# Optimization experiments

Hardware: AMD Instinct MI355X
Metric: run time of the kernel (lower is better)

Reference implementation:

```python
import jax, jax.numpy as jnp
import numpy as np

C = 1.0          # ball curvature c (manifold k = -c)
RC = 1.0         # sqrt(c)
PROJ_EPS = 4e-3  # geoopt float32 projection eps
NUM_HEADS = 16
B, S, D = 2, 1024, 1024


def _project(x):
    # clip points back inside the Poincare ball
    maxnorm = (1.0 - PROJ_EPS) / RC
    norm = jnp.maximum(jnp.linalg.norm(x, axis=-1, keepdims=True), 1e-15)
    return jnp.where(norm > maxnorm, x / norm * maxnorm, x)


def _poincare_linear(x, z, r, out_split):
    # Unidirectional Poincare MLR (Shimizu et al., HNN++) followed by exp-map back to the ball.
    # x: [..., din]; z: [din, dout]; r: [dout]
    z_norm = jnp.maximum(jnp.linalg.norm(z, axis=0, keepdims=True), 1e-15)  # [1, dout]
    z_unit = z / z_norm
    drcr = 2.0 * RC * r                                    # [dout]
    rcx = RC * x
    cx2 = jnp.sum(rcx * rcx, axis=-1, keepdims=True)       # [..., 1]
    w = 2.0 * (z_norm / RC) * jnp.arcsinh(
        (2.0 * (rcx @ z_unit) * jnp.cosh(drcr) - (1.0 + cx2) * jnp.sinh(drcr))
        / jnp.maximum(1.0 - cx2, 1e-15))
    y = jnp.sinh(RC * w) / RC
    y = y.reshape(y.shape[:-1] + (out_split, y.shape[-1] // out_split))  # [..., H, dh]
    y = _project(y)
    y = y / (1.0 + jnp.sqrt(1.0 + C * jnp.sum(y * y, axis=-1, keepdims=True)))
    return _project(y)


def _dist_matmul(x, y):
    # Pairwise Poincare distance via matmul. x: [..., n, d], y: [..., d, m].
    # dist = (1/sqrt(c)) * arccosh(1 + 2c||x-y||^2 / ((1-c||x||^2)(1-c||y||^2)))
    xy = jnp.matmul(x, y)
    x2 = jnp.sum(x * x, axis=-1, keepdims=True)           # [..., n, 1]
    y2 = jnp.sum(y * y, axis=-2, keepdims=True)           # [..., 1, m]
    num = jnp.maximum(x2 - 2.0 * xy + y2, 1e-15)          # ||x - y||^2
    den = jnp.maximum((1.0 - C * x2) * (1.0 - C * y2), 1e-15)
    return (1.0 / RC) * jnp.arccosh(1.0 + 2.0 * C * num / den)


def _weighted_midpoint_bmm(xs, weights):
    # Weighted Mobius gyromidpoint. xs: [..., n, d], weights: [..., m, n] -> [..., m, d]
    x2 = jnp.sum(xs * xs, axis=-1, keepdims=True)
    gamma = 2.0 / jnp.maximum(1.0 - C * x2, 1e-15)        # conformal factor lambda_x
    denom = jnp.matmul(jnp.abs(weights), gamma - 1.0)     # [..., m, 1]
    nomin = jnp.matmul(weights, gamma * xs)               # [..., m, d]
    two_mean = nomin / jnp.maximum(denom, 1e-10)
    sq = jnp.sum(two_mean * two_mean, axis=-1, keepdims=True)
    a_mean = two_mean / (1.0 + jnp.sqrt(jnp.maximum(1.0 - C * sq, 1e-15)))
    return _project(a_mean)


def setup_inputs() -> dict:
    key = jax.random.key(0)
    ks = jax.random.split(key, 4)
    # points must lie inside the unit ball: ||x|| ~ 0.02*sqrt(D) ~ 0.64
    hidden_states = 0.02 * jax.random.normal(ks[0], (B, S, D), dtype=jnp.float32)
    attention_mask = jnp.zeros((B, 1, 1, S), dtype=jnp.float32)
    scale = 1.0 / np.sqrt(D).astype(np.float32)
    qz = scale * jax.random.normal(ks[1], (D, D), dtype=jnp.float32)
    kz = scale * jax.random.normal(ks[2], (D, D), dtype=jnp.float32)
    vz = scale * jax.random.normal(ks[3], (D, D), dtype=jnp.float32)
    qr = jnp.zeros((D,), jnp.float32)
    kr = jnp.zeros((D,), jnp.float32)
    vr = jnp.zeros((D,), jnp.float32)
    return {"hidden_states": hidden_states, "attention_mask": attention_mask,
            "qz": qz, "qr": qr, "kz": kz, "kr": kr, "vz": vz, "vr": vr}


def reference(hidden_states, attention_mask, qz, qr, kz, kr, vz, vr):
    # self-attention path (encoder_hidden_states is None), eval mode (dropout p=0)
    q = _poincare_linear(hidden_states, qz, qr, NUM_HEADS).transpose(0, 2, 1, 3)  # [B,H,S,dh]
    k = _poincare_linear(hidden_states, kz, kr, NUM_HEADS).transpose(0, 2, 1, 3)
    v = _poincare_linear(hidden_states, vz, vr, NUM_HEADS).transpose(0, 2, 1, 3)
    scores = -_dist_matmul(q, jnp.swapaxes(k, -1, -2)) + attention_mask          # [B,H,S,S]
    probs = jax.nn.softmax(scores, axis=-1)
    ctx = _weighted_midpoint_bmm(v, probs)                                       # [B,H,S,dh]
    b, h, s, dh = ctx.shape
    return ctx.transpose(0, 2, 1, 3).reshape(b, s, h * dh)
```

## Files before the change

### kernel.cpp

```cpp
#include <hip/hip_runtime.h>
#include <math.h>

#define BB 2
#define SS 1024
#define DD 1024
#define NH 16
#define DH 64
#define MAXN 0.996f

typedef __attribute__((ext_vector_type(8))) short bf16x8;
typedef __attribute__((ext_vector_type(4))) float f32x4;

__device__ __forceinline__ float xor_sum16(float v){
  v += __shfl_xor(v, 1, 64);
  v += __shfl_xor(v, 2, 64);
  v += __shfl_xor(v, 4, 64);
  v += __shfl_xor(v, 8, 64);
  return v;
}

__device__ __forceinline__ unsigned short f2bf(float x){
  unsigned u = __builtin_bit_cast(unsigned, x);
  unsigned r = u + 0x7FFFu + ((u >> 16) & 1u);
  return (unsigned short)(r >> 16);
}
__device__ __forceinline__ float bf2f(unsigned short b){
  unsigned u = ((unsigned)b) << 16;
  return __builtin_bit_cast(float, u);
}

__device__ __forceinline__ void async_copy16(const unsigned short* g, unsigned short* s){
  __builtin_amdgcn_global_load_lds(
      (const __attribute__((address_space(1))) unsigned int*)g,
      (__attribute__((address_space(3))) unsigned int*)s,
      16, 0, 0);
}

__global__ __launch_bounds__(256) void prep_kernel(
    const float* __restrict__ hs,
    const float* __restrict__ zq, const float* __restrict__ zk, const float* __restrict__ zv,
    float* __restrict__ cx2, float* __restrict__ partial,
    unsigned short* __restrict__ Xhi, unsigned short* __restrict__ Xlo,
    unsigned short* __restrict__ ZThi, unsigned short* __restrict__ ZTlo)
{
  __shared__ unsigned shbuf[64 * 69];
  __shared__ float csred[4][64];
  const int bid = blockIdx.x;
  const int tid = threadIdx.x;

  if (bid < 1024) {
    const int b = bid;
    const size_t g0 = (size_t)b * 2048 + (size_t)tid * 8;
    float acc = 0.0f;
    #pragma unroll
    for (int h = 0; h < 2; ++h) {
      float4 v = *(const float4*)(hs + g0 + 4 * h);
      float a[4] = {v.x, v.y, v.z, v.w};
      ushort4 hv, lv;
      unsigned short* hp = (unsigned short*)&hv;
      unsigned short* lp = (unsigned short*)&lv;
      #pragma unroll
      for (int j = 0; j < 4; ++j) {
        acc = fmaf(a[j], a[j], acc);
        unsigned short hi = f2bf(a[j]);
        hp[j] = hi;
        lp[j] = f2bf(a[j] - bf2f(hi));
      }
      *(ushort4*)(Xhi + g0 + 4 * h) = hv;
      *(ushort4*)(Xlo + g0 + 4 * h) = lv;
    }
    #pragma unroll
    for (int m = 1; m < 64; m <<= 1) acc += __shfl_xor(acc, m, 64);
    float* red = (float*)shbuf;
    const int wave = tid >> 6, lane = tid & 63;
    if (lane == 0) red[wave] = acc;
    __syncthreads();
    if (tid == 0)   cx2[2 * b]     = red[0] + red[1];
    if (tid == 128) cx2[2 * b + 1] = red[2] + red[3];
  } else {
    const int b2 = bid - 1024;
    const int kt = b2 & 15, nt = (b2 >> 4) & 15, mat = b2 >> 8;
    const float* z = (mat == 0) ? zq : ((mat == 1) ? zk : zv);
    const int wave = tid >> 6, lane = tid & 63;
    unsigned (*T)[69] = (unsigned(*)[69])shbuf;
    float cs[4] = {0.f, 0.f, 0.f, 0.f};
    #pragma unroll
    for (int i = 0; i < 4; ++i) {
      const int g = tid + 256 * i;
      const int kr = g >> 4, nc = (g & 15) * 4;
      float4 v = *(const float4*)(z + (size_t)(kt * 64 + kr) * DD + nt * 64 + nc);
      float a[4] = {v.x, v.y, v.z, v.w};
      #pragma unroll
      for (int j = 0; j < 4; ++j) {
        cs[j] = fmaf(a[j], a[j], cs[j]);
        unsigned short hi = f2bf(a[j]);
        unsigned short lo = f2bf(a[j] - bf2f(hi));
        T[kr][nc + j] = ((unsigned)lo << 16) | (unsigned)hi;
      }
    }
    #pragma unroll
    for (int j = 0; j < 4; ++j) {
      cs[j] += __shfl_xor(cs[j], 16, 64);
      cs[j] += __shfl_xor(cs[j], 32, 64);
    }
    if (lane < 16) {
      #pragma unroll
      for (int j = 0; j < 4; ++j) csred[wave][lane * 4 + j] = cs[j];
    }
    __syncthreads();
    #pragma unroll
    for (int i = 0; i < 4; ++i) {
      const int g = tid + 256 * i;
      const int nr = g >> 4, kc = (g & 15) * 4;
      ushort4 hv, lv;
      unsigned short* hp = (unsigned short*)&hv;
      unsigned short* lp = (unsigned short*)&lv;
      #pragma unroll
      for (int j = 0; j < 4; ++j) {
        unsigned u = T[kc + j][nr];
        hp[j] = (unsigned short)(u & 0xFFFFu);
        lp[j] = (unsigned short)(u >> 16);
      }
      const size_t ob = ((size_t)mat * DD + nt * 64 + nr) * DD + kt * 64 + kc;
      *(ushort4*)(ZThi + ob) = hv;
      *(ushort4*)(ZTlo + ob) = lv;
    }
    if (tid < 64) {
      float s = csred[0][tid] + csred[1][tid] + csred[2][tid] + csred[3][tid];
      partial[kt * 3072 + mat * DD + nt * 64 + tid] = s;
    }
  }
}

__global__ __launch_bounds__(256) void colstats_finalize_kernel(
    const float* __restrict__ partial,
    const float* __restrict__ rq, const float* __restrict__ rk, const float* __restrict__ rv,
    float* __restrict__ acol, float* __restrict__ bcol, float* __restrict__ scol)
{
  const int col = blockIdx.x * 256 + threadIdx.x;
  float s = 0.f;
  #pragma unroll
  for (int rc = 0; rc < 16; ++rc) s += partial[rc * 3072 + col];
  const int m = col >> 10, c = col & 1023;
  const float* r = (m == 0) ? rq : ((m == 1) ? rk : rv);
  const float n = fmaxf(sqrtf(s), 1e-15f);
  const float rr = 2.0f * r[c];
  acol[col] = 2.0f * coshf(rr) / n;
  bcol[col] = sinhf(rr);
  scol[col] = 2.0f * n;
}

__global__ __launch_bounds__(256, 2) void gemm_mfma_kernel(
    const unsigned short* __restrict__ Xhi, const unsigned short* __restrict__ Xlo,
    const unsigned short* __restrict__ ZThi, const unsigned short* __restrict__ ZTlo,
    const float* __restrict__ acol, const float* __restrict__ bcol, const float* __restrict__ scol,
    const float* __restrict__ cx2,
    unsigned short* __restrict__ Qhi, unsigned short* __restrict__ Qlo,
    unsigned short* __restrict__ Khi, unsigned short* __restrict__ Klo,
    unsigned short* __restrict__ GThi, unsigned short* __restrict__ GTlo,
    float* __restrict__ q2, float* __restrict__ k2, float* __restrict__ gm1)
{
  __shared__ __align__(16) unsigned char shmem[66560];
  unsigned short* Sbuf = (unsigned short*)shmem;

  const int mat = blockIdx.z;
  float* Stat = (mat == 0) ? q2 : ((mat == 1) ? k2 : gm1);
  unsigned short* Bh = (mat == 0) ? Qhi : Khi;
  unsigned short* Bl = (mat == 0) ? Qlo : Klo;

  const int n0 = blockIdx.x * 128;
  const int m0 = blockIdx.y * 128;
  const int tid = threadIdx.x;
  const int wave = tid >> 6, lane = tid & 63;
  const int tx = lane & 15, quad = lane >> 4;
  const int wrow = wave >> 1;
  const int wcol = wave & 1;

  const int l4r = lane >> 2;
  const int l4c = 8 * (((lane & 3) - (l4r >> 1)) & 3);
  const unsigned short* abase =
      (wave == 0) ? Xhi : (wave == 1) ? Xlo : (wave == 2) ? ZThi : ZTlo;
  const size_t rowbase = (wave < 2) ? (size_t)m0 : (size_t)(mat * DD + n0);
  const unsigned short* P[8];
  #pragma unroll
  for (int i = 0; i < 8; ++i)
    P[i] = abase + (rowbase + i * 16 + l4r) * DD + l4c;
  const int ldsw = 4096 * wave;

  const int koff = 8 * ((quad + (tx >> 1)) & 3);

  const f32x4 z4 = {0.f, 0.f, 0.f, 0.f};
  f32x4 acc[4][4];
  #pragma unroll
  for (int mb = 0; mb < 4; ++mb)
    #pragma unroll
    for (int nb = 0; nb < 4; ++nb) acc[mb][nb] = z4;

  #pragma unroll
  for (int i = 0; i < 8; ++i) {
    async_copy16(P[i], Sbuf + ldsw + 512 * i);
    P[i] += 32;
  }

  for (int kt = 0; kt < 32; ++kt) {
    __syncthreads();
    if (kt < 31) {
      unsigned short* Bn = Sbuf + 16384 * ((kt + 1) & 1);
      #pragma unroll
      for (int i = 0; i < 8; ++i) {
        async_copy16(P[i], Bn + ldsw + 512 * i);
        P[i] += 32;
      }
    }
    const unsigned short* Bc = Sbuf + 16384 * (kt & 1);

    bf16x8 a_h[4], a_l[4];
    #pragma unroll
    for (int mb = 0; mb < 4; ++mb) {
      const int ar = 64 * wrow + 16 * mb + tx;
      a_h[mb] = *(const bf16x8*)&Bc[ar * 32 + koff];
      a_l[mb] = *(const bf16x8*)&Bc[4096 + ar * 32 + koff];
    }
    #pragma unroll
    for (int nb = 0; nb < 4; ++nb) {
      const int br = 64 * wcol + 16 * nb + tx;
      bf16x8 b_h = *(const bf16x8*)&Bc[8192 + br * 32 + koff];
      bf16x8 b_l = *(const bf16x8*)&Bc[12288 + br * 32 + koff];
      #pragma unroll
      for (int mb = 0; mb < 4; ++mb)
        acc[mb][nb] = __builtin_amdgcn_mfma_f32_16x16x32_bf16(a_h[mb], b_h, acc[mb][nb], 0, 0, 0);
      #pragma unroll
      for (int mb = 0; mb < 4; ++mb)
        acc[mb][nb] = __builtin_amdgcn_mfma_f32_16x16x32_bf16(a_h[mb], b_l, acc[mb][nb], 0, 0, 0);
      #pragma unroll
      for (int mb = 0; mb < 4; ++mb)
        acc[mb][nb] = __builtin_amdgcn_mfma_f32_16x16x32_bf16(a_l[mb], b_h, acc[mb][nb], 0, 0, 0);
    }
  }

  const int head = blockIdx.x * 2 + wcol;
  unsigned* Tr = (unsigned*)shmem;
  if (mat == 2) __syncthreads();

  #pragma unroll
  for (int mb = 0; mb < 4; ++mb) {
    #pragma unroll
    for (int r = 0; r < 4; ++r) {
      const int sl = 64 * wrow + 16 * mb + 4 * quad + r;
      const int row = m0 + sl;
      const float c2 = cx2[row];
      const float inv = 1.0f / fmaxf(1.0f - c2, 1e-15f);
      const float onec = 1.0f + c2;
      float yv[4];
      #pragma unroll
      for (int nb = 0; nb < 4; ++nb) {
        const float accv = acc[mb][nb][r];
        const int col = mat * DD + n0 + 64 * wcol + 16 * nb + tx;
        const float u = fmaf(accv, acol[col], -(onec * bcol[col])) * inv;
        const float a = fabsf(u);
        const float t = a + sqrtf(fmaf(a, a, 1.0f));
        const float p = __builtin_amdgcn_exp2f(scol[col] * __builtin_amdgcn_logf(t));
        float y = 0.5f * (p - __builtin_amdgcn_rcpf(p));
        yv[nb] = copysignf(y, u);
      }
      const int b = row >> 10, s = row & 1023;
      float n2 = 0.f;
      #pragma unroll
      for (int j = 0; j < 4; ++j) n2 = fmaf(yv[j], yv[j], n2);
      n2 = xor_sum16(n2);
      float n = fmaxf(sqrtf(n2), 1e-15f);
      float s1 = (n > MAXN) ? (MAXN / n) : 1.0f;
      n2 = n2 * s1 * s1;
      float f = 1.0f / (1.0f + sqrtf(1.0f + n2));
      float fs = s1 * f;
      n2 = n2 * f * f;
      float nb2 = fmaxf(sqrtf(n2), 1e-15f);
      float s2f = (nb2 > MAXN) ? (MAXN / nb2) : 1.0f;
      fs *= s2f;
      n2 = n2 * s2f * s2f;

      const size_t bh = (size_t)(b * NH + head);
      const size_t outbase = (bh * SS + s) * DH;
      if (mat == 2) {
        const float gamma = 2.0f / fmaxf(1.0f - n2, 1e-15f);
        #pragma unroll
        for (int j = 0; j < 4; ++j) {
          const float v = yv[j] * fs * gamma;
          const unsigned short hi = f2bf(v);
          const unsigned short lo = f2bf(v - bf2f(hi));
          Tr[(wcol * 128 + sl) * 65 + 16 * j + tx] = ((unsigned)lo << 16) | (unsigned)hi;
        }
        if (tx == 0) Stat[bh * SS + s] = gamma - 1.0f;
      } else {
        #pragma unroll
        for (int j = 0; j < 4; ++j) {
          const float v = yv[j] * fs;
          const unsigned short hi = f2bf(v);
          const unsigned short lo = f2bf(v - bf2f(hi));
          Bh[outbase + 16 * j + tx] = hi;
          Bl[outbase + 16 * j + tx] = lo;
        }
        if (tx == 0) Stat[bh * SS + s] = n2;
      }
    }
  }

  if (mat == 2) {
    __syncthreads();
    const int bb = m0 >> 10, sbase = m0 & 1023;
    #pragma unroll
    for (int i = 0; i < 4; ++i) {
      const int task = tid + 256 * i;
      const int rowid = task >> 3;
      const int hh = rowid >> 6, dh = rowid & 63;
      const int sc = (task & 7) * 16;
      unsigned short hbuf[16] __attribute__((aligned(16)));
      unsigned short lbuf[16] __attribute__((aligned(16)));
      #pragma unroll
      for (int s = 0; s < 16; ++s) {
        unsigned u = Tr[(hh * 128 + sc + s) * 65 + dh];
        hbuf[s] = (unsigned short)(u & 0xFFFFu);
        lbuf[s] = (unsigned short)(u >> 16);
      }
      const int hg = blockIdx.x * 2 + hh;
      const size_t ob = (((size_t)(bb * NH + hg)) * DH + dh) * SS + sbase + sc;
      *(uint4*)(GThi + ob)     = *(uint4*)&hbuf[0];
      *(uint4*)(GThi + ob + 8) = *(uint4*)&hbuf[8];
      *(uint4*)(GTlo + ob)     = *(uint4*)&lbuf[0];
      *(uint4*)(GTlo + ob + 8) = *(uint4*)&lbuf[8];
    }
  }
}

__global__ __launch_bounds__(256) void flash_attn_kernel(
    const unsigned short* __restrict__ Qhi, const unsigned short* __restrict__ Qlo,
    const unsigned short* __restrict__ Khi, const unsigned short* __restrict__ Klo,
    const unsigned short* __restrict__ GThi, const unsigned short* __restrict__ GTlo,
    const float* __restrict__ q2a, const float* __restrict__ k2a, const float* __restrict__ gm1a,
    const float* __restrict__ mask, float* __restrict__ out)
{
  __shared__ unsigned short Ksh[2][2048];
  __shared__ unsigned short Ksl[2][2048];
  __shared__ unsigned short Gsh[2][2048];
  __shared__ unsigned short Gsl[2][2048];
  __shared__ unsigned short Psh[64 * 40];
  __shared__ unsigned short Psl[64 * 40];
  __shared__ float k2s[2][32], ik2s[2][32], gm1s[2][32], ems[2][32];

  const int h = blockIdx.x, qt = blockIdx.y, b = blockIdx.z;
  const int bh = b * NH + h;
  const int tid = threadIdx.x;
  const int wave = tid >> 6, lane = tid & 63;
  const int tx = lane & 15, quad = lane >> 4;
  const int r0 = qt * 64;

  bf16x8 qa_h[2], qa_l[2];
  {
    const size_t qoff = ((size_t)bh * SS + r0 + 16 * wave + tx) * DH;
    #pragma unroll
    for (int kc = 0; kc < 2; ++kc) {
      qa_h[kc] = *(const bf16x8*)(Qhi + qoff + 32 * kc + 8 * quad);
      qa_l[kc] = *(const bf16x8*)(Qlo + qoff + 32 * kc + 8 * quad);
    }
  }
  float q2r[4], iq2[4];
  #pragma unroll
  for (int r = 0; r < 4; ++r) {
    q2r[r] = q2a[(size_t)bh * SS + r0 + 16 * wave + 4 * quad + r];
    iq2[r] = 2.0f / fmaxf(1.0f - q2r[r], 1e-15f);
  }

  const f32x4 zero4 = {0.f, 0.f, 0.f, 0.f};
  f32x4 oacc[4] = {zero4, zero4, zero4, zero4};
  float dden[4] = {0.f, 0.f, 0.f, 0.f};

  const size_t kbase = (size_t)bh * SS * DH;
  const size_t gbase = (size_t)bh * DH * SS;

  const unsigned short* sArr =
      (wave == 0) ? Khi : (wave == 1) ? Klo : (wave == 2) ? GThi : GTlo;
  const unsigned short* sBase = sArr + ((wave < 2) ? kbase : gbase);
  const int tAdv = (wave < 2) ? 32 * DH : 32;
  int srcoff[4];
  if (wave < 2) {
    #pragma unroll
    for (int i = 0; i < 4; ++i) {
      const int r = 8 * i + (lane >> 3);
      srcoff[i] = r * DH + 8 * (((lane & 7) - r) & 7);
    }
  } else {
    #pragma unroll
    for (int i = 0; i < 4; ++i) {
      const int r = 16 * i + (lane >> 2);
      srcoff[i] = r * SS + 8 * (((lane & 3) - r) & 3);
    }
  }
  unsigned short* ldsDst[2];
  ldsDst[0] = (wave == 0) ? Ksh[0] : (wave == 1) ? Ksl[0] : (wave == 2) ? Gsh[0] : Gsl[0];
  ldsDst[1] = (wave == 0) ? Ksh[1] : (wave == 1) ? Ksl[1] : (wave == 2) ? Gsh[1] : Gsl[1];

  float s_k2 = 0.f, s_gm1 = 0.f, s_ms = 0.f;

  {
    const unsigned short* s = sBase;
    #pragma unroll
    for (int i = 0; i < 4; ++i) async_copy16(s + srcoff[i], ldsDst[0] + i * 512);
  }
  if (tid < 32) {
    s_k2  = k2a[(size_t)bh * SS + tid];
    s_gm1 = gm1a[(size_t)bh * SS + tid];
    s_ms  = mask[(size_t)b * SS + tid];
    k2s[0][tid]  = s_k2;
    ik2s[0][tid] = 1.0f / fmaxf(1.0f - s_k2, 1e-15f);
    gm1s[0][tid] = s_gm1;
    ems[0][tid]  = __expf(s_ms);
    s_k2  = k2a[(size_t)bh * SS + 32 + tid];
    s_gm1 = gm1a[(size_t)bh * SS + 32 + tid];
    s_ms  = mask[(size_t)b * SS + 32 + tid];
  }

  for (int kt = 0; kt < 32; ++kt) {
    __syncthreads();
    if (kt < 31) {
      const int nbuf = (kt + 1) & 1;
      const unsigned short* s = sBase + (size_t)(kt + 1) * tAdv;
      #pragma unroll
      for (int i = 0; i < 4; ++i) async_copy16(s + srcoff[i], ldsDst[nbuf] + i * 512);
      if (tid < 32) {
        k2s[nbuf][tid]  = s_k2;
        ik2s[nbuf][tid] = 1.0f / fmaxf(1.0f - s_k2, 1e-15f);
        gm1s[nbuf][tid] = s_gm1;
        ems[nbuf][tid]  = __expf(s_ms);
        if (kt < 30) {
          const int t2 = (kt + 2) * 32;
          s_k2  = k2a[(size_t)bh * SS + t2 + tid];
          s_gm1 = gm1a[(size_t)bh * SS + t2 + tid];
          s_ms  = mask[(size_t)b * SS + t2 + tid];
        }
      }
    }
    const int cb = kt & 1;

    f32x4 sacc[2] = {zero4, zero4};
    #pragma unroll
    for (int kc = 0; kc < 2; ++kc) {
      #pragma unroll
      for (int nb = 0; nb < 2; ++nb) {
        const int row = 16 * nb + tx;
        const int off = row * 64 + 8 * (((4 * kc + quad) + row) & 7);
        bf16x8 kh = *(const bf16x8*)&Ksh[cb][off];
        bf16x8 kl = *(const bf16x8*)&Ksl[cb][off];
        sacc[nb] = __builtin_amdgcn_mfma_f32_16x16x32_bf16(qa_h[kc], kh, sacc[nb], 0, 0, 0);
        sacc[nb] = __builtin_amdgcn_mfma_f32_16x16x32_bf16(qa_h[kc], kl, sacc[nb], 0, 0, 0);
        sacc[nb] = __builtin_amdgcn_mfma_f32_16x16x32_bf16(qa_l[kc], kh, sacc[nb], 0, 0, 0);
      }
    }

    float pb[4][2];
    #pragma unroll
    for (int nb = 0; nb < 2; ++nb) {
      const int key = 16 * nb + tx;
      const float k2v = k2s[cb][key], ikv = ik2s[cb][key], emv = ems[cb][key], gmv = gm1s[cb][key];
      #pragma unroll
      for (int r = 0; r < 4; ++r) {
        float sv = sacc[nb][r];
        float num = fmaxf(fmaf(-2.0f, sv, q2r[r] + k2v), 1e-15f);
        float e = num * iq2[r] * ikv;
        float g = fmaf(e, e, e + e);
        float z = 1.0f + e + __builtin_amdgcn_sqrtf(g);
        float w = emv * __builtin_amdgcn_rcpf(z);
        pb[r][nb] = w;
        dden[r] = fmaf(w, gmv, dden[r]);
      }
    }

    #pragma unroll
    for (int r = 0; r < 4; ++r) {
      const int prow = 16 * wave + 4 * quad + r;
      #pragma unroll
      for (int nb = 0; nb < 2; ++nb) {
        float w = pb[r][nb];
        unsigned short hi = f2bf(w);
        unsigned short lo = f2bf(w - bf2f(hi));
        Psh[prow * 40 + 16 * nb + tx] = hi;
        Psl[prow * 40 + 16 * nb + tx] = lo;
      }
    }
    bf16x8 ph = *(const bf16x8*)&Psh[(16 * wave + tx) * 40 + 8 * quad];
    bf16x8 pl = *(const bf16x8*)&Psl[(16 * wave + tx) * 40 + 8 * quad];
    #pragma unroll
    for (int nb = 0; nb < 4; ++nb) {
      const int row = 16 * nb + tx;
      const int off = row * 32 + 8 * ((quad + row) & 3);
      bf16x8 gh = *(const bf16x8*)&Gsh[cb][off];
      bf16x8 gl = *(const bf16x8*)&Gsl[cb][off];
      oacc[nb] = __builtin_amdgcn_mfma_f32_16x16x32_bf16(ph, gh, oacc[nb], 0, 0, 0);
      oacc[nb] = __builtin_amdgcn_mfma_f32_16x16x32_bf16(ph, gl, oacc[nb], 0, 0, 0);
      oacc[nb] = __builtin_amdgcn_mfma_f32_16x16x32_bf16(pl, gh, oacc[nb], 0, 0, 0);
    }
  }

  #pragma unroll
  for (int r = 0; r < 4; ++r) {
    float d = fmaxf(xor_sum16(dden[r]), 1e-10f);
    float invd = 1.0f / d;
    float tm[4]; float sq = 0.f;
    #pragma unroll
    for (int nb = 0; nb < 4; ++nb) { tm[nb] = oacc[nb][r] * invd; sq = fmaf(tm[nb], tm[nb], sq); }
    sq = xor_sum16(sq);
    const float f = 1.0f / (1.0f + sqrtf(fmaxf(1.0f - sq, 1e-15f)));
    const float n2 = sq * f * f;
    const float n = fmaxf(sqrtf(n2), 1e-15f);
    const float s2 = (n > MAXN) ? (MAXN / n) : 1.0f;
    const float fs = f * s2;
    const int qrow = r0 + 16 * wave + 4 * quad + r;
    #pragma unroll
    for (int nb = 0; nb < 4; ++nb)
      out[((size_t)(b * SS + qrow)) * DD + h * DH + 16 * nb + tx] = tm[nb] * fs;
  }
}

extern "C" void kernel_launch(void* const* d_in, const int* in_sizes, int n_in,
                              void* d_out, int out_size, void* d_ws, size_t ws_size,
                              hipStream_t stream) {
  const float* hs   = (const float*)d_in[0];
  const float* mask = (const float*)d_in[1];
  const float* qz   = (const float*)d_in[2];
  const float* qr   = (const float*)d_in[3];
  const float* kz   = (const float*)d_in[4];
  const float* kr   = (const float*)d_in[5];
  const float* vz   = (const float*)d_in[6];
  const float* vr   = (const float*)d_in[7];
  float* out = (float*)d_out;

  float* ws = (float*)d_ws;
  const size_t nQKV = (size_t)BB * NH * SS * DH;
  const size_t nStat = (size_t)BB * NH * SS;

  float* q2  = ws;
  float* k2  = q2 + nStat;
  float* gm1 = k2 + nStat;
  float* acol = gm1 + nStat;
  float* bcol = acol + 3 * DD;
  float* scol = bcol + 3 * DD;
  float* cx2 = scol + 3 * DD;
  float* partial = cx2 + 2048;

  unsigned short* sb   = (unsigned short*)(partial + 16 * 3072);
  unsigned short* Qhi  = sb;
  unsigned short* Qlo  = Qhi + nQKV;
  unsigned short* Khi  = Qlo + nQKV;
  unsigned short* Klo  = Khi + nQKV;
  unsigned short* GThi = Klo + nQKV;
  unsigned short* GTlo = GThi + nQKV;
  unsigned short* Xhi  = GTlo + nQKV;
  unsigned short* Xlo  = Xhi + nQKV;
  unsigned short* ZThi = Xlo + nQKV;
  unsigned short* ZTlo = ZThi + 3 * (size_t)DD * DD;

  prep_kernel<<<dim3(1792), 256, 0, stream>>>(
      hs, qz, kz, vz, cx2, partial, Xhi, Xlo, ZThi, ZTlo);
  colstats_finalize_kernel<<<dim3(12), 256, 0, stream>>>(
      partial, qr, kr, vr, acol, bcol, scol);
  gemm_mfma_kernel<<<dim3(8, 16, 3), 256, 0, stream>>>(
      Xhi, Xlo, ZThi, ZTlo, acol, bcol, scol, cx2,
      Qhi, Qlo, Khi, Klo, GThi, GTlo, q2, k2, gm1);
  flash_attn_kernel<<<dim3(NH, 16, BB), 256, 0, stream>>>(
      Qhi, Qlo, Khi, Klo, GThi, GTlo, q2, k2, gm1, mask, out);
}
```

Baseline: 200.2 us.

## Fuse GEMM and flash attention into one cooperative kernel with grid sync

Drops the separate column-stats finalize kernel by computing the per-column coefficients inside the GEMM epilogue. The GEMM and attention stages are merged into one cooperative launch of 512 blocks that does a grid-wide sync between them, with a fallback to two separate launches if the cooperative launch fails. The aim is to remove launch overheads and inter-kernel gaps. In exchange, every GEMM block now redundantly re-reads the partial sums, and the attention phase runs with the GEMM's larger shared-memory footprint and occupancy bound of 2 blocks per CU.

```diff
diff --git a/kernel.cpp b/kernel.cpp
--- a/kernel.cpp
+++ b/kernel.cpp
@@ -1,5 +1,8 @@
 #include <hip/hip_runtime.h>
+#include <hip/hip_cooperative_groups.h>
 #include <math.h>
+
+namespace cg = cooperative_groups;
 
 #define BB 2
 #define SS 1024
@@ -132,44 +135,26 @@
   }
 }
 
-__global__ __launch_bounds__(256) void colstats_finalize_kernel(
+__device__ __forceinline__ void gemm_body(
+    int bx, int by, int mat, unsigned char* shmem,
+    const unsigned short* __restrict__ Xhi, const unsigned short* __restrict__ Xlo,
+    const unsigned short* __restrict__ ZThi, const unsigned short* __restrict__ ZTlo,
     const float* __restrict__ partial,
     const float* __restrict__ rq, const float* __restrict__ rk, const float* __restrict__ rv,
-    float* __restrict__ acol, float* __restrict__ bcol, float* __restrict__ scol)
-{
-  const int col = blockIdx.x * 256 + threadIdx.x;
-  float s = 0.f;
-  #pragma unroll
-  for (int rc = 0; rc < 16; ++rc) s += partial[rc * 3072 + col];
-  const int m = col >> 10, c = col & 1023;
-  const float* r = (m == 0) ? rq : ((m == 1) ? rk : rv);
-  const float n = fmaxf(sqrtf(s), 1e-15f);
-  const float rr = 2.0f * r[c];
-  acol[col] = 2.0f * coshf(rr) / n;
-  bcol[col] = sinhf(rr);
-  scol[col] = 2.0f * n;
-}
-
-__global__ __launch_bounds__(256, 2) void gemm_mfma_kernel(
-    const unsigned short* __restrict__ Xhi, const unsigned short* __restrict__ Xlo,
-    const unsigned short* __restrict__ ZThi, const unsigned short* __restrict__ ZTlo,
-    const float* __restrict__ acol, const float* __restrict__ bcol, const float* __restrict__ scol,
     const float* __restrict__ cx2,
     unsigned short* __restrict__ Qhi, unsigned short* __restrict__ Qlo,
     unsigned short* __restrict__ Khi, unsigned short* __restrict__ Klo,
     unsigned short* __restrict__ GThi, unsigned short* __restrict__ GTlo,
     float* __restrict__ q2, float* __restrict__ k2, float* __restrict__ gm1)
 {
-  __shared__ __align__(16) unsigned char shmem[66560];
   unsigned short* Sbuf = (unsigned short*)shmem;
 
-  const int mat = blockIdx.z;
   float* Stat = (mat == 0) ? q2 : ((mat == 1) ? k2 : gm1);
   unsigned short* Bh = (mat == 0) ? Qhi : Khi;
   unsigned short* Bl = (mat == 0) ? Qlo : Klo;
 
-  const int n0 = blockIdx.x * 128;
-  const int m0 = blockIdx.y * 128;
+  const int n0 = bx * 128;
+  const int m0 = by * 128;
   const int tid = threadIdx.x;
   const int wave = tid >> 6, lane = tid & 63;
   const int tx = lane & 15, quad = lane >> 4;
@@ -238,7 +223,25 @@
     }
   }
 
-  const int head = blockIdx.x * 2 + wcol;
+  float acolv[4], bcolv[4], scolv[4];
+  {
+    const float* rarr = (mat == 0) ? rq : ((mat == 1) ? rk : rv);
+    #pragma unroll
+    for (int nb = 0; nb < 4; ++nb) {
+      const int c = n0 + 64 * wcol + 16 * nb + tx;
+      const int colg = mat * DD + c;
+      float s = 0.f;
+      #pragma unroll
+      for (int rc = 0; rc < 16; ++rc) s += partial[rc * 3072 + colg];
+      const float n = fmaxf(sqrtf(s), 1e-15f);
+      const float rr2 = 2.0f * rarr[c];
+      acolv[nb] = 2.0f * coshf(rr2) / n;
+      bcolv[nb] = sinhf(rr2);
+      scolv[nb] = 2.0f * n;
+    }
+  }
+
+  const int head = bx * 2 + wcol;
   unsigned* Tr = (unsigned*)shmem;
   if (mat == 2) __syncthreads();
 
@@ -255,11 +258,10 @@
       #pragma unroll
       for (int nb = 0; nb < 4; ++nb) {
         const float accv = acc[mb][nb][r];
-        const int col = mat * DD + n0 + 64 * wcol + 16 * nb + tx;
-        const float u = fmaf(accv, acol[col], -(onec * bcol[col])) * inv;
+        const float u = fmaf(accv, acolv[nb], -(onec * bcolv[nb])) * inv;
         const float a = fabsf(u);
         const float t = a + sqrtf(fmaf(a, a, 1.0f));
-        const float p = __builtin_amdgcn_exp2f(scol[col] * __builtin_amdgcn_logf(t));
+        const float p = __builtin_amdgcn_exp2f(scolv[nb] * __builtin_amdgcn_logf(t));
         float y = 0.5f * (p - __builtin_amdgcn_rcpf(p));
         yv[nb] = copysignf(y, u);
       }
@@ -322,7 +324,7 @@
         hbuf[s] = (unsigned short)(u & 0xFFFFu);
         lbuf[s] = (unsigned short)(u >> 16);
       }
-      const int hg = blockIdx.x * 2 + hh;
+      const int hg = bx * 2 + hh;
       const size_t ob = (((size_t)(bb * NH + hg)) * DH + dh) * SS + sbase + sc;
       *(uint4*)(GThi + ob)     = *(uint4*)&hbuf[0];
       *(uint4*)(GThi + ob + 8) = *(uint4*)&hbuf[8];
@@ -332,22 +334,27 @@
   }
 }
 
-__global__ __launch_bounds__(256) void flash_attn_kernel(
+__device__ __forceinline__ void flash_body(
+    int h, int qt, int b, unsigned char* shmem,
     const unsigned short* __restrict__ Qhi, const unsigned short* __restrict__ Qlo,
     const unsigned short* __restrict__ Khi, const unsigned short* __restrict__ Klo,
     const unsigned short* __restrict__ GThi, const unsigned short* __restrict__ GTlo,
     const float* __restrict__ q2a, const float* __restrict__ k2a, const float* __restrict__ gm1a,
     const float* __restrict__ mask, float* __restrict__ out)
 {
-  __shared__ unsigned short Ksh[2][2048];
-  __shared__ unsigned short Ksl[2][2048];
-  __shared__ unsigned short Gsh[2][2048];
-  __shared__ unsigned short Gsl[2][2048];
-  __shared__ unsigned short Psh[64 * 40];
-  __shared__ unsigned short Psl[64 * 40];
-  __shared__ float k2s[2][32], ik2s[2][32], gm1s[2][32], ems[2][32];
-
-  const int h = blockIdx.x, qt = blockIdx.y, b = blockIdx.z;
+  unsigned short* S16 = (unsigned short*)shmem;
+  unsigned short* Ksh = S16;
+  unsigned short* Ksl = S16 + 4096;
+  unsigned short* Gsh = S16 + 8192;
+  unsigned short* Gsl = S16 + 12288;
+  unsigned short* Psh = S16 + 16384;
+  unsigned short* Psl = S16 + 18944;
+  float* fst  = (float*)(shmem + 43008);
+  float* k2s  = fst;
+  float* ik2s = fst + 64;
+  float* gm1s = fst + 128;
+  float* ems  = fst + 192;
+
   const int bh = b * NH + h;
   const int tid = threadIdx.x;
   const int wave = tid >> 6, lane = tid & 63;
@@ -396,8 +403,8 @@
     }
   }
   unsigned short* ldsDst[2];
-  ldsDst[0] = (wave == 0) ? Ksh[0] : (wave == 1) ? Ksl[0] : (wave == 2) ? Gsh[0] : Gsl[0];
-  ldsDst[1] = (wave == 0) ? Ksh[1] : (wave == 1) ? Ksl[1] : (wave == 2) ? Gsh[1] : Gsl[1];
+  ldsDst[0] = (wave == 0) ? Ksh : (wave == 1) ? Ksl : (wave == 2) ? Gsh : Gsl;
+  ldsDst[1] = ldsDst[0] + 2048;
 
   float s_k2 = 0.f, s_gm1 = 0.f, s_ms = 0.f;
 
@@ -410,10 +417,10 @@
     s_k2  = k2a[(size_t)bh * SS + tid];
     s_gm1 = gm1a[(size_t)bh * SS + tid];
     s_ms  = mask[(size_t)b * SS + tid];
-    k2s[0][tid]  = s_k2;
-    ik2s[0][tid] = 1.0f / fmaxf(1.0f - s_k2, 1e-15f);
-    gm1s[0][tid] = s_gm1;
-    ems[0][tid]  = __expf(s_ms);
+    k2s[tid]  = s_k2;
+    ik2s[tid] = 1.0f / fmaxf(1.0f - s_k2, 1e-15f);
+    gm1s[tid] = s_gm1;
+    ems[tid]  = __expf(s_ms);
     s_k2  = k2a[(size_t)bh * SS + 32 + tid];
     s_gm1 = gm1a[(size_t)bh * SS + 32 + tid];
     s_ms  = mask[(size_t)b * SS + 32 + tid];
@@ -427,10 +434,10 @@
       #pragma unroll
       for (int i = 0; i < 4; ++i) async_copy16(s + srcoff[i], ldsDst[nbuf] + i * 512);
       if (tid < 32) {
-        k2s[nbuf][tid]  = s_k2;
-        ik2s[nbuf][tid] = 1.0f / fmaxf(1.0f - s_k2, 1e-15f);
-        gm1s[nbuf][tid] = s_gm1;
-        ems[nbuf][tid]  = __expf(s_ms);
+        k2s[nbuf * 32 + tid]  = s_k2;
+        ik2s[nbuf * 32 + tid] = 1.0f / fmaxf(1.0f - s_k2, 1e-15f);
+        gm1s[nbuf * 32 + tid] = s_gm1;
+        ems[nbuf * 32 + tid]  = __expf(s_ms);
         if (kt < 30) {
           const int t2 = (kt + 2) * 32;
           s_k2  = k2a[(size_t)bh * SS + t2 + tid];
@@ -448,8 +455,8 @@
       for (int nb = 0; nb < 2; ++nb) {
         const int row = 16 * nb + tx;
         const int off = row * 64 + 8 * (((4 * kc + quad) + row) & 7);
-        bf16x8 kh = *(const bf16x8*)&Ksh[cb][off];
-        bf16x8 kl = *(const bf16x8*)&Ksl[cb][off];
+        bf16x8 kh = *(const bf16x8*)&Ksh[cb * 2048 + off];
+        bf16x8 kl = *(const bf16x8*)&Ksl[cb * 2048 + off];
         sacc[nb] = __builtin_amdgcn_mfma_f32_16x16x32_bf16(qa_h[kc], kh, sacc[nb], 0, 0, 0);
         sacc[nb] = __builtin_amdgcn_mfma_f32_16x16x32_bf16(qa_h[kc], kl, sacc[nb], 0, 0, 0);
         sacc[nb] = __builtin_amdgcn_mfma_f32_16x16x32_bf16(qa_l[kc], kh, sacc[nb], 0, 0, 0);
@@ -460,7 +467,8 @@
     #pragma unroll
     for (int nb = 0; nb < 2; ++nb) {
       const int key = 16 * nb + tx;
-      const float k2v = k2s[cb][key], ikv = ik2s[cb][key], emv = ems[cb][key], gmv = gm1s[cb][key];
+      const float k2v = k2s[cb * 32 + key], ikv = ik2s[cb * 32 + key];
+      const float emv = ems[cb * 32 + key], gmv = gm1s[cb * 32 + key];
       #pragma unroll
       for (int r = 0; r < 4; ++r) {
         float sv = sacc[nb][r];
@@ -492,8 +500,8 @@
     for (int nb = 0; nb < 4; ++nb) {
       const int row = 16 * nb + tx;
       const int off = row * 32 + 8 * ((quad + row) & 3);
-      bf16x8 gh = *(const bf16x8*)&Gsh[cb][off];
-      bf16x8 gl = *(const bf16x8*)&Gsl[cb][off];
+      bf16x8 gh = *(const bf16x8*)&Gsh[cb * 2048 + off];
+      bf16x8 gl = *(const bf16x8*)&Gsl[cb * 2048 + off];
       oacc[nb] = __builtin_amdgcn_mfma_f32_16x16x32_bf16(ph, gh, oacc[nb], 0, 0, 0);
       oacc[nb] = __builtin_amdgcn_mfma_f32_16x16x32_bf16(ph, gl, oacc[nb], 0, 0, 0);
       oacc[nb] = __builtin_amdgcn_mfma_f32_16x16x32_bf16(pl, gh, oacc[nb], 0, 0, 0);
@@ -518,6 +526,60 @@
     for (int nb = 0; nb < 4; ++nb)
       out[((size_t)(b * SS + qrow)) * DD + h * DH + 16 * nb + tx] = tm[nb] * fs;
   }
+}
+
+__global__ __launch_bounds__(256, 2) void gemm_mfma_kernel(
+    const unsigned short* __restrict__ Xhi, const unsigned short* __restrict__ Xlo,
+    const unsigned short* __restrict__ ZThi, const unsigned short* __restrict__ ZTlo,
+    const float* __restrict__ partial,
+    const float* __restrict__ rq, const float* __restrict__ rk, const float* __restrict__ rv,
+    const float* __restrict__ cx2,
+    unsigned short* __restrict__ Qhi, unsigned short* __restrict__ Qlo,
+    unsigned short* __restrict__ Khi, unsigned short* __restrict__ Klo,
+    unsigned short* __restrict__ GThi, unsigned short* __restrict__ GTlo,
+    float* __restrict__ q2, float* __restrict__ k2, float* __restrict__ gm1)
+{
+  __shared__ __align__(16) unsigned char shmem[66560];
+  gemm_body(blockIdx.x, blockIdx.y, blockIdx.z, shmem,
+            Xhi, Xlo, ZThi, ZTlo, partial, rq, rk, rv, cx2,
+            Qhi, Qlo, Khi, Klo, GThi, GTlo, q2, k2, gm1);
+}
+
+__global__ __launch_bounds__(256) void flash_attn_kernel(
+    const unsigned short* __restrict__ Qhi, const unsigned short* __restrict__ Qlo,
+    const unsigned short* __restrict__ Khi, const unsigned short* __restrict__ Klo,
+    const unsigned short* __restrict__ GThi, const unsigned short* __restrict__ GTlo,
+    const float* __restrict__ q2a, const float* __restrict__ k2a, const float* __restrict__ gm1a,
+    const float* __restrict__ mask, float* __restrict__ out)
+{
+  __shared__ __align__(16) unsigned char shmem[44032];
+  flash_body(blockIdx.x, blockIdx.y, blockIdx.z, shmem,
+             Qhi, Qlo, Khi, Klo, GThi, GTlo, q2a, k2a, gm1a, mask, out);
+}
+
+__global__ __launch_bounds__(256, 2) void gemm_flash_kernel(
+    const unsigned short* __restrict__ Xhi, const unsigned short* __restrict__ Xlo,
+    const unsigned short* __restrict__ ZThi, const unsigned short* __restrict__ ZTlo,
+    const float* __restrict__ partial,
+    const float* __restrict__ rq, const float* __restrict__ rk, const float* __restrict__ rv,
+    const float* __restrict__ cx2,
+    unsigned short* __restrict__ Qhi, unsigned short* __restrict__ Qlo,
+    unsigned short* __restrict__ Khi, unsigned short* __restrict__ Klo,
+    unsigned short* __restrict__ GThi, unsigned short* __restrict__ GTlo,
+    float* __restrict__ q2, float* __restrict__ k2, float* __restrict__ gm1,
+    const float* __restrict__ mask, float* __restrict__ out)
+{
+  __shared__ __align__(16) unsigned char shmem[66560];
+  const int bid = blockIdx.x;
+
+  if (bid < 384) {
+    gemm_body(bid & 7, (bid >> 3) & 15, bid >> 7, shmem,
+              Xhi, Xlo, ZThi, ZTlo, partial, rq, rk, rv, cx2,
+              Qhi, Qlo, Khi, Klo, GThi, GTlo, q2, k2, gm1);
+  }
+  cg::this_grid().sync();
+  flash_body(bid & 15, (bid >> 4) & 15, bid >> 8, shmem,
+             Qhi, Qlo, Khi, Klo, GThi, GTlo, q2, k2, gm1, mask, out);
 }
 
 extern "C" void kernel_launch(void* const* d_in, const int* in_sizes, int n_in,
@@ -540,10 +602,7 @@
   float* q2  = ws;
   float* k2  = q2 + nStat;
   float* gm1 = k2 + nStat;
-  float* acol = gm1 + nStat;
-  float* bcol = acol + 3 * DD;
-  float* scol = bcol + 3 * DD;
-  float* cx2 = scol + 3 * DD;
+  float* cx2 = gm1 + nStat;
   float* partial = cx2 + 2048;
 
   unsigned short* sb   = (unsigned short*)(partial + 16 * 3072);
@@ -560,11 +619,21 @@
 
   prep_kernel<<<dim3(1792), 256, 0, stream>>>(
       hs, qz, kz, vz, cx2, partial, Xhi, Xlo, ZThi, ZTlo);
-  colstats_finalize_kernel<<<dim3(12), 256, 0, stream>>>(
-      partial, qr, kr, vr, acol, bcol, scol);
-  gemm_mfma_kernel<<<dim3(8, 16, 3), 256, 0, stream>>>(
-      Xhi, Xlo, ZThi, ZTlo, acol, bcol, scol, cx2,
-      Qhi, Qlo, Khi, Klo, GThi, GTlo, q2, k2, gm1);
-  flash_attn_kernel<<<dim3(NH, 16, BB), 256, 0, stream>>>(
-      Qhi, Qlo, Khi, Klo, GThi, GTlo, q2, k2, gm1, mask, out);
-}
+
+  void* kargs[] = {
+      (void*)&Xhi, (void*)&Xlo, (void*)&ZThi, (void*)&ZTlo, (void*)&partial,
+      (void*)&qr, (void*)&kr, (void*)&vr, (void*)&cx2,
+      (void*)&Qhi, (void*)&Qlo, (void*)&Khi, (void*)&Klo,
+      (void*)&GThi, (void*)&GTlo, (void*)&q2, (void*)&k2, (void*)&gm1,
+      (void*)&mask, (void*)&out};
+  hipError_t e = hipLaunchCooperativeKernel(
+      (const void*)gemm_flash_kernel, dim3(512), dim3(256), kargs, 0, stream);
+  if (e != hipSuccess) {
+    (void)hipGetLastError();
+    gemm_mfma_kernel<<<dim3(8, 16, 3), 256, 0, stream>>>(
+        Xhi, Xlo, ZThi, ZTlo, partial, qr, kr, vr, cx2,
+        Qhi, Qlo, Khi, Klo, GThi, GTlo, q2, k2, gm1);
+    flash_attn_kernel<<<dim3(NH, 16, BB), 256, 0, stream>>>(
+        Qhi, Qlo, Khi, Klo, GThi, GTlo, q2, k2, gm1, mask, out);
+  }
+}
```

Result: slower. 274.2 us (+37.0%).
